# Kernel tuning notes

Hardware: AMD Instinct MI355X
Metric: run time of the kernel (lower is better)

Reference implementation:

```python
import jax, jax.numpy as jnp
import numpy as np

C = 256        # conv_dim / hidden_size
VOC = 106      # voc_size + 1
MAX_LEN = 25   # num_chars
GROUPS = 32


def setup_inputs() -> dict:
    key = jax.random.key(0)
    ks = jax.random.split(key, 32)
    s = 0.05
    d = {}
    d['rois'] = jax.random.normal(ks[0], (64, C, 16, 128), jnp.float32)
    d['conv1_w'] = jax.random.normal(ks[1], (C, C, 3, 3), jnp.float32) * s
    d['gn1_g'] = jnp.ones((C,), jnp.float32)
    d['gn1_b'] = jnp.zeros((C,), jnp.float32)
    d['conv2_w'] = jax.random.normal(ks[2], (C, C, 3, 3), jnp.float32) * s
    d['gn2_g'] = jnp.ones((C,), jnp.float32)
    d['gn2_b'] = jnp.zeros((C,), jnp.float32)
    # BiLSTM (nIn=C, nHidden=C), PyTorch gate order i,f,g,o
    d['lstm_wih_f'] = jax.random.normal(ks[3], (4 * C, C), jnp.float32) * s
    d['lstm_whh_f'] = jax.random.normal(ks[4], (4 * C, C), jnp.float32) * s
    d['lstm_bih_f'] = jnp.zeros((4 * C,), jnp.float32)
    d['lstm_bhh_f'] = jnp.zeros((4 * C,), jnp.float32)
    d['lstm_wih_b'] = jax.random.normal(ks[5], (4 * C, C), jnp.float32) * s
    d['lstm_whh_b'] = jax.random.normal(ks[6], (4 * C, C), jnp.float32) * s
    d['lstm_bih_b'] = jnp.zeros((4 * C,), jnp.float32)
    d['lstm_bhh_b'] = jnp.zeros((4 * C,), jnp.float32)
    d['emb_w'] = jax.random.normal(ks[7], (C, 2 * C), jnp.float32) * s   # 2H -> C projection
    d['emb_b'] = jnp.zeros((C,), jnp.float32)
    # Attention decoder params
    d['att_emb'] = jax.random.normal(ks[8], (VOC, C), jnp.float32) * s   # char embedding table
    d['comb_w'] = jax.random.normal(ks[9], (C, 2 * C), jnp.float32) * s  # attn_combine
    d['comb_b'] = jnp.zeros((C,), jnp.float32)
    d['gru_wih'] = jax.random.normal(ks[10], (3 * C, C), jnp.float32) * s  # gates r,z,n
    d['gru_whh'] = jax.random.normal(ks[11], (3 * C, C), jnp.float32) * s
    d['gru_bih'] = jnp.zeros((3 * C,), jnp.float32)
    d['gru_bhh'] = jnp.zeros((3 * C,), jnp.float32)
    d['out_w'] = jax.random.normal(ks[12], (VOC, C), jnp.float32) * s
    d['out_b'] = jnp.zeros((VOC,), jnp.float32)
    d['vat_w'] = jax.random.normal(ks[13], (1, C), jnp.float32) * s
    d['vat_b'] = jnp.zeros((1,), jnp.float32)
    return d


def _group_norm(x, g, b, eps=1e-5):
    N, Ch, H, W = x.shape
    xg = x.reshape(N, GROUPS, Ch // GROUPS, H, W)
    m = xg.mean(axis=(2, 3, 4), keepdims=True)
    v = xg.var(axis=(2, 3, 4), keepdims=True)
    xn = ((xg - m) / jnp.sqrt(v + eps)).reshape(N, Ch, H, W)
    return xn * g[None, :, None, None] + b[None, :, None, None]


def _conv_gn_relu(x, w, g, b):
    y = jax.lax.conv_general_dilated(x, w, window_strides=(2, 1),
                                     padding=((1, 1), (1, 1)),
                                     dimension_numbers=('NCHW', 'OIHW', 'NCHW'))
    return jax.nn.relu(_group_norm(y, g, b))


def _lstm_dir(x, Wih, Whh, bih, bhh, reverse):
    # x: (T, N, C) -> hidden states (T, N, H)
    N = x.shape[1]
    Hd = Whh.shape[1]
    def step(carry, xt):
        h, c = carry
        gates = xt @ Wih.T + h @ Whh.T + (bih + bhh)
        i, f, gg, o = jnp.split(gates, 4, axis=-1)
        c = jax.nn.sigmoid(f) * c + jax.nn.sigmoid(i) * jnp.tanh(gg)
        h = jax.nn.sigmoid(o) * jnp.tanh(c)
        return (h, c), h
    init = (jnp.zeros((N, Hd), x.dtype), jnp.zeros((N, Hd), x.dtype))
    _, hs = jax.lax.scan(step, init, x, reverse=reverse)
    return hs


def _forward(rois, conv1_w, gn1_g, gn1_b, conv2_w, gn2_g, gn2_b,
             lstm_wih_f, lstm_whh_f, lstm_bih_f, lstm_bhh_f,
             lstm_wih_b, lstm_whh_b, lstm_bih_b, lstm_bhh_b,
             emb_w, emb_b, att_emb, comb_w, comb_b,
             gru_wih, gru_whh, gru_bih, gru_bhh, out_w, out_b, vat_w, vat_b):
    # CRNN encoder
    x = _conv_gn_relu(rois, conv1_w, gn1_g, gn1_b)
    x = _conv_gn_relu(x, conv2_w, gn2_g, gn2_b)
    x = x.mean(axis=2)                      # (N, C, W)
    x = jnp.transpose(x, (2, 0, 1))         # (T, N, C)
    fw = _lstm_dir(x, lstm_wih_f, lstm_whh_f, lstm_bih_f, lstm_bhh_f, False)
    bw = _lstm_dir(x, lstm_wih_b, lstm_whh_b, lstm_bih_b, lstm_bhh_b, True)
    rec = jnp.concatenate([fw, bw], axis=-1)        # (T, N, 2C)
    enc = rec @ emb_w.T + emb_b                     # (T, N, C) encoder_outputs

    n = enc.shape[1]

    def dec_step(carry, _):
        inp, h = carry                              # inp: (n,) int, h: (n, C)
        e = att_emb[inp]                            # embedding (dropout = identity at eval)
        alpha = jnp.tanh(h[None, :, :] + enc)       # (T, n, C)
        aw = jnp.squeeze(alpha @ vat_w.T, -1) + vat_b[0]  # (T, n)
        aw = jax.nn.softmax(aw, axis=0)             # softmax over time
        ctx = jnp.einsum('tn,tnc->nc', aw, enc)     # attn_applied
        o = jax.nn.relu(jnp.concatenate([e, ctx], axis=-1) @ comb_w.T + comb_b)
        gi = o @ gru_wih.T + gru_bih
        gh = h @ gru_whh.T + gru_bhh
        ir, iz, innw = jnp.split(gi, 3, axis=-1)
        hr, hz, hn = jnp.split(gh, 3, axis=-1)
        r = jax.nn.sigmoid(ir + hr)
        z = jax.nn.sigmoid(iz + hz)
        nn_ = jnp.tanh(innw + r * hn)
        h2 = (1.0 - z) * nn_ + z * h
        logits = jax.nn.log_softmax(h2 @ out_w.T + out_b, axis=-1)
        ni = jnp.argmax(logits, axis=-1)            # greedy feedback
        return (ni, h2), logits

    init = (jnp.zeros((n,), jnp.int32), jnp.zeros((n, C), enc.dtype))
    _, outs = jax.lax.scan(dec_step, init, None, length=MAX_LEN)
    return jnp.transpose(outs, (1, 0, 2))           # decoder_raw: (n, MAX_LEN, VOC)


def reference(rois, conv1_w, gn1_g, gn1_b, conv2_w, gn2_g, gn2_b,
              lstm_wih_f, lstm_whh_f, lstm_bih_f, lstm_bhh_f,
              lstm_wih_b, lstm_whh_b, lstm_bih_b, lstm_bhh_b,
              emb_w, emb_b, att_emb, comb_w, comb_b,
              gru_wih, gru_whh, gru_bih, gru_bhh, out_w, out_b, vat_w, vat_b):
    return _forward(rois, conv1_w, gn1_g, gn1_b, conv2_w, gn2_g, gn2_b,
                    lstm_wih_f, lstm_whh_f, lstm_bih_f, lstm_bhh_f,
                    lstm_wih_b, lstm_whh_b, lstm_bih_b, lstm_bhh_b,
                    emb_w, emb_b, att_emb, comb_w, comb_b,
                    gru_wih, gru_whh, gru_bih, gru_bhh, out_w, out_b, vat_w, vat_b)
```

## Files before the change

kernel.cpp:

```cpp
#include <hip/hip_runtime.h>
#include <cstdint>

typedef unsigned short u16;
typedef unsigned int   u32;
typedef __attribute__((ext_vector_type(8))) __bf16 bf16x8;
typedef __attribute__((ext_vector_type(4))) float  f32x4;

#define DEV static __device__ __forceinline__

DEV float bf2f(u16 u) { union { u32 i; float f; } v; v.i = ((u32)u) << 16; return v.f; }
DEV u16 f2bf(float f) {
  union { float f; u32 i; } v; v.f = f;
  u32 x = v.i;
  x += 0x7fffu + ((x >> 16) & 1u);
  return (u16)(x >> 16);
}
DEV void splitf(float x, u16 &h, u16 &l) { h = f2bf(x); float r = x - bf2f(h); l = f2bf(r); }
DEV float sigm(float x) { return 1.f / (1.f + __expf(-x)); }
DEV float tanh_(float x) { float e = __expf(2.f * x); return 1.f - 2.f / (e + 1.f); }
DEV f32x4 mfma_bf16(bf16x8 a, bf16x8 b, f32x4 c) {
  return __builtin_amdgcn_mfma_f32_16x16x32_bf16(a, b, c, 0, 0, 0);
}

__global__ __launch_bounds__(256) void k_repack_convw(const float* __restrict__ w,
                                                      u16* __restrict__ oh, u16* __restrict__ ol) {
  int idx = blockIdx.x * 256 + threadIdx.x;
  if (idx >= 256 * 2304) return;
  int co = idx / 2304, r = idx - co * 2304;
  int seg = r >> 8, ci = r & 255;
  float v = w[(co * 256 + ci) * 9 + seg];
  u16 h, l; splitf(v, h, l);
  oh[idx] = h; ol[idx] = l;
}

__global__ __launch_bounds__(256) void k_split(const float* __restrict__ s,
                                               u16* __restrict__ h, u16* __restrict__ l, int count) {
  int i = blockIdx.x * 256 + threadIdx.x;
  if (i < count) { u16 a, b; splitf(s[i], a, b); h[i] = a; l[i] = b; }
}

template <int H_OUT, int H_IN, int MODE>
__global__ __launch_bounds__(256)
void k_conv_gemm(const float* __restrict__ Ain, const u16* __restrict__ Bth, const u16* __restrict__ Btl,
                 float* __restrict__ Out, const float* __restrict__ gstat,
                 const float* __restrict__ gamma, const float* __restrict__ beta) {
  __shared__ __align__(16) u16 Ash[128 * 32];
  __shared__ __align__(16) u16 Asl[128 * 32];
  __shared__ __align__(16) u16 Bsh[128 * 32];
  __shared__ __align__(16) u16 Bsl[128 * 32];
  const int tid = threadIdx.x;
  const int bx = blockIdx.x, ct = blockIdx.y;
  const int n = bx / H_OUT, hp = bx % H_OUT;
  const int wid = tid >> 6, lane = tid & 63;
  const int wr = wid >> 1, wc = wid & 1;
  const int lr = lane & 15, lk = lane >> 4;
  const int iw = tid & 127, chalf = tid >> 7;
  f32x4 acc[4][4] = {};
  for (int step = 0; step < 72; ++step) {
    const int seg = step >> 3, ci0 = (step & 7) << 5;
    const int kh = seg / 3, kw = seg - kh * 3;
    const int ih = 2 * hp + kh - 1;
    const int iws = iw + kw - 1;
    const bool ok = (ih >= 0) && (ih < H_IN) && (iws >= 0) && (iws < 128);
#pragma unroll
    for (int j = 0; j < 2; ++j) {
      int chunk = j * 256 + tid;
      int row = chunk >> 2, sub = chunk & 3;
      int off = (ct * 128 + row) * 2304 + step * 32 + sub * 8;
      *(uint4*)&Bsh[chunk * 8] = *(const uint4*)&Bth[off];
      *(uint4*)&Bsl[chunk * 8] = *(const uint4*)&Btl[off];
    }
    if constexpr (MODE == 0) {
      const float* src = Ain + (((long)(n * 256 + ci0) * H_IN + ih) * 128 + iws);
#pragma unroll
      for (int g8 = 0; g8 < 2; ++g8) {
        u32 ph[4], pl[4];
#pragma unroll
        for (int q = 0; q < 4; ++q) {
          int c = chalf * 16 + g8 * 8 + q * 2;
          float v0 = 0.f, v1 = 0.f;
          if (ok) { v0 = src[(long)c * (H_IN * 128)]; v1 = src[(long)(c + 1) * (H_IN * 128)]; }
          u16 h0, l0, h1, l1; splitf(v0, h0, l0); splitf(v1, h1, l1);
          ph[q] = (u32)h0 | ((u32)h1 << 16);
          pl[q] = (u32)l0 | ((u32)l1 << 16);
        }
        *(uint4*)&Ash[iw * 32 + chalf * 16 + g8 * 8] = make_uint4(ph[0], ph[1], ph[2], ph[3]);
        *(uint4*)&Asl[iw * 32 + chalf * 16 + g8 * 8] = make_uint4(pl[0], pl[1], pl[2], pl[3]);
      }
    } else {
      const float* src = Ain + ((((long)n * H_IN + ih) * 128 + iws) * 256 + ci0 + chalf * 16);
#pragma unroll
      for (int g8 = 0; g8 < 2; ++g8) {
        int c0 = ci0 + chalf * 16 + g8 * 8;
        int g = c0 >> 3;
        float m = gstat[(n * 32 + g) * 2], rs = gstat[(n * 32 + g) * 2 + 1];
        float x[8] = {};
        if (ok) {
          float4 a = *(const float4*)(src + g8 * 8);
          float4 b = *(const float4*)(src + g8 * 8 + 4);
          x[0] = a.x; x[1] = a.y; x[2] = a.z; x[3] = a.w;
          x[4] = b.x; x[5] = b.y; x[6] = b.z; x[7] = b.w;
        }
        u32 ph[4], pl[4];
#pragma unroll
        for (int q = 0; q < 4; ++q) {
          int c = c0 + q * 2;
          float v0 = ok ? fmaxf((x[q * 2]     - m) * rs * gamma[c]     + beta[c],     0.f) : 0.f;
          float v1 = ok ? fmaxf((x[q * 2 + 1] - m) * rs * gamma[c + 1] + beta[c + 1], 0.f) : 0.f;
          u16 h0, l0, h1, l1; splitf(v0, h0, l0); splitf(v1, h1, l1);
          ph[q] = (u32)h0 | ((u32)h1 << 16);
          pl[q] = (u32)l0 | ((u32)l1 << 16);
        }
        *(uint4*)&Ash[iw * 32 + chalf * 16 + g8 * 8] = make_uint4(ph[0], ph[1], ph[2], ph[3]);
        *(uint4*)&Asl[iw * 32 + chalf * 16 + g8 * 8] = make_uint4(pl[0], pl[1], pl[2], pl[3]);
      }
    }
    __syncthreads();
    bf16x8 ah[4], al[4], bh[4], bl[4];
#pragma unroll
    for (int mi = 0; mi < 4; ++mi) {
      int row = wr * 64 + mi * 16 + lr;
      ah[mi] = *(const bf16x8*)&Ash[row * 32 + lk * 8];
      al[mi] = *(const bf16x8*)&Asl[row * 32 + lk * 8];
    }
#pragma unroll
    for (int ni = 0; ni < 4; ++ni) {
      int row = wc * 64 + ni * 16 + lr;
      bh[ni] = *(const bf16x8*)&Bsh[row * 32 + lk * 8];
      bl[ni] = *(const bf16x8*)&Bsl[row * 32 + lk * 8];
    }
#pragma unroll
    for (int mi = 0; mi < 4; ++mi)
#pragma unroll
      for (int ni = 0; ni < 4; ++ni) {
        f32x4 c = acc[mi][ni];
        c = mfma_bf16(al[mi], bh[ni], c);
        c = mfma_bf16(ah[mi], bl[ni], c);
        c = mfma_bf16(ah[mi], bh[ni], c);
        acc[mi][ni] = c;
      }
    __syncthreads();
  }
#pragma unroll
  for (int mi = 0; mi < 4; ++mi)
#pragma unroll
    for (int ni = 0; ni < 4; ++ni)
#pragma unroll
      for (int r = 0; r < 4; ++r) {
        int w = wr * 64 + mi * 16 + lk * 4 + r;
        int co = ct * 128 + wc * 64 + ni * 16 + lr;
        Out[(((long)(n * H_OUT + hp)) * 128 + w) * 256 + co] = acc[mi][ni][r];
      }
}

__global__ __launch_bounds__(256)
void k_gemm_split(const u16* __restrict__ Ah, const u16* __restrict__ Al,
                  const u16* __restrict__ Bh, const u16* __restrict__ Bl,
                  float* __restrict__ outF, const float* __restrict__ bias, int K) {
  __shared__ __align__(16) u16 Ash[128 * 32];
  __shared__ __align__(16) u16 Asl[128 * 32];
  __shared__ __align__(16) u16 Bsh[128 * 32];
  __shared__ __align__(16) u16 Bsl[128 * 32];
  const int tid = threadIdx.x;
  const int m0 = blockIdx.x * 128, n0 = blockIdx.y * 128;
  const int N = gridDim.y * 128;
  const int wid = tid >> 6, lane = tid & 63;
  const int wr = wid >> 1, wc = wid & 1;
  const int lr = lane & 15, lk = lane >> 4;
  f32x4 acc[4][4] = {};
  const int steps = K >> 5;
  for (int s = 0; s < steps; ++s) {
    const int k0 = s << 5;
#pragma unroll
    for (int j = 0; j < 2; ++j) {
      int chunk = j * 256 + tid;
      int row = chunk >> 2, sub = chunk & 3;
      long aoff = (long)(m0 + row) * K + k0 + sub * 8;
      long boff = (long)(n0 + row) * K + k0 + sub * 8;
      *(uint4*)&Ash[chunk * 8] = *(const uint4*)&Ah[aoff];
      *(uint4*)&Asl[chunk * 8] = *(const uint4*)&Al[aoff];
      *(uint4*)&Bsh[chunk * 8] = *(const uint4*)&Bh[boff];
      *(uint4*)&Bsl[chunk * 8] = *(const uint4*)&Bl[boff];
    }
    __syncthreads();
    bf16x8 ah[4], al[4], bh[4], bl[4];
#pragma unroll
    for (int mi = 0; mi < 4; ++mi) {
      int row = wr * 64 + mi * 16 + lr;
      ah[mi] = *(const bf16x8*)&Ash[row * 32 + lk * 8];
      al[mi] = *(const bf16x8*)&Asl[row * 32 + lk * 8];
    }
#pragma unroll
    for (int ni = 0; ni < 4; ++ni) {
      int row = wc * 64 + ni * 16 + lr;
      bh[ni] = *(const bf16x8*)&Bsh[row * 32 + lk * 8];
      bl[ni] = *(const bf16x8*)&Bsl[row * 32 + lk * 8];
    }
#pragma unroll
    for (int mi = 0; mi < 4; ++mi)
#pragma unroll
      for (int ni = 0; ni < 4; ++ni) {
        f32x4 c = acc[mi][ni];
        c = mfma_bf16(al[mi], bh[ni], c);
        c = mfma_bf16(ah[mi], bl[ni], c);
        c = mfma_bf16(ah[mi], bh[ni], c);
        acc[mi][ni] = c;
      }
    __syncthreads();
  }
#pragma unroll
  for (int mi = 0; mi < 4; ++mi)
#pragma unroll
    for (int ni = 0; ni < 4; ++ni)
#pragma unroll
      for (int r = 0; r < 4; ++r) {
        int m = m0 + wr * 64 + mi * 16 + lk * 4 + r;
        int col = n0 + wc * 64 + ni * 16 + lr;
        float v = acc[mi][ni][r];
        if (bias) v += bias[col];
        outF[(long)m * N + col] = v;
      }
}

__global__ __launch_bounds__(256)
void k_gemm_gx(const u16* __restrict__ Ah, const u16* __restrict__ Al,
               const u16* __restrict__ Bh, const u16* __restrict__ Bl,
               float* __restrict__ outF) {
  __shared__ __align__(16) u16 Ash[128 * 32];
  __shared__ __align__(16) u16 Asl[128 * 32];
  __shared__ __align__(16) u16 Bsh[128 * 32];
  __shared__ __align__(16) u16 Bsl[128 * 32];
  const int tid = threadIdx.x;
  const int m0 = blockIdx.x * 128, n0 = blockIdx.y * 128;
  const int K = 256;
  const int wid = tid >> 6, lane = tid & 63;
  const int wr = wid >> 1, wc = wid & 1;
  const int lr = lane & 15, lk = lane >> 4;
  f32x4 acc[4][4] = {};
  for (int s = 0; s < 8; ++s) {
    const int k0 = s << 5;
#pragma unroll
    for (int j = 0; j < 2; ++j) {
      int chunk = j * 256 + tid;
      int row = chunk >> 2, sub = chunk & 3;
      long aoff = (long)(m0 + row) * K + k0 + sub * 8;
      long boff = (long)(n0 + row) * K + k0 + sub * 8;
      *(uint4*)&Ash[chunk * 8] = *(const uint4*)&Ah[aoff];
      *(uint4*)&Asl[chunk * 8] = *(const uint4*)&Al[aoff];
      *(uint4*)&Bsh[chunk * 8] = *(const uint4*)&Bh[boff];
      *(uint4*)&Bsl[chunk * 8] = *(const uint4*)&Bl[boff];
    }
    __syncthreads();
    bf16x8 ah[4], al[4], bh[4], bl[4];
#pragma unroll
    for (int mi = 0; mi < 4; ++mi) {
      int row = wr * 64 + mi * 16 + lr;
      ah[mi] = *(const bf16x8*)&Ash[row * 32 + lk * 8];
      al[mi] = *(const bf16x8*)&Asl[row * 32 + lk * 8];
    }
#pragma unroll
    for (int ni = 0; ni < 4; ++ni) {
      int row = wc * 64 + ni * 16 + lr;
      bh[ni] = *(const bf16x8*)&Bsh[row * 32 + lk * 8];
      bl[ni] = *(const bf16x8*)&Bsl[row * 32 + lk * 8];
    }
#pragma unroll
    for (int mi = 0; mi < 4; ++mi)
#pragma unroll
      for (int ni = 0; ni < 4; ++ni) {
        f32x4 c = acc[mi][ni];
        c = mfma_bf16(al[mi], bh[ni], c);
        c = mfma_bf16(ah[mi], bl[ni], c);
        c = mfma_bf16(ah[mi], bh[ni], c);
        acc[mi][ni] = c;
      }
    __syncthreads();
  }
#pragma unroll
  for (int mi = 0; mi < 4; ++mi)
#pragma unroll
    for (int ni = 0; ni < 4; ++ni) {
      int t = blockIdx.x * 2 + wr;
      int nbase = mi * 16 + lk * 4;
      int col = n0 + wc * 64 + ni * 16 + lr;
      int gate = col >> 8, u = col & 255;
      int prow = ((u >> 4) << 6) + (gate << 4) + (u & 15);
      float4 st = make_float4(acc[mi][ni][0], acc[mi][ni][1], acc[mi][ni][2], acc[mi][ni][3]);
      *(float4*)&outF[((long)t * 1024 + prow) * 64 + nbase] = st;
    }
}

__global__ __launch_bounds__(256)
void k_gn_stats(const float* __restrict__ y, float* __restrict__ stat, int H) {
  const int n = blockIdx.x >> 5, g = blockIdx.x & 31;
  const int tid = threadIdx.x;
  const int cnt = H * 128;
  float s = 0.f, q = 0.f;
  for (int i = tid; i < cnt; i += 256) {
    int h = i >> 7, w = i & 127;
    const float4* p = (const float4*)(y + (((long)(n * H + h) * 128 + w) * 256 + g * 8));
    float4 a = p[0], b = p[1];
    s += a.x + a.y + a.z + a.w + b.x + b.y + b.z + b.w;
    q += a.x * a.x + a.y * a.y + a.z * a.z + a.w * a.w + b.x * b.x + b.y * b.y + b.z * b.z + b.w * b.w;
  }
  __shared__ float rs_[256], rq_[256];
  rs_[tid] = s; rq_[tid] = q; __syncthreads();
  for (int off = 128; off > 0; off >>= 1) {
    if (tid < off) { rs_[tid] += rs_[tid + off]; rq_[tid] += rq_[tid + off]; }
    __syncthreads();
  }
  if (tid == 0) {
    float c = (float)(cnt * 8);
    float m = rs_[0] / c;
    float var = rq_[0] / c - m * m;
    stat[(n * 32 + g) * 2] = m;
    stat[(n * 32 + g) * 2 + 1] = rsqrtf(var + 1e-5f);
  }
}

__global__ __launch_bounds__(256)
void k_xbuild(const float* __restrict__ out2, const float* __restrict__ stat,
              const float* __restrict__ gamma, const float* __restrict__ beta,
              u16* __restrict__ xh, u16* __restrict__ xl) {
  int idx = blockIdx.x * 256 + threadIdx.x;
  int c = idx & 255;
  int n = (idx >> 8) & 63;
  int t = idx >> 14;
  int g = c >> 3;
  float m = stat[(n * 32 + g) * 2], rs = stat[(n * 32 + g) * 2 + 1];
  float ga = gamma[c], be = beta[c];
  float acc = 0.f;
#pragma unroll
  for (int h = 0; h < 4; ++h) {
    float v = out2[(((long)(n * 4 + h) * 128 + t) * 256) + c];
    acc += fmaxf((v - m) * rs * ga + be, 0.f);
  }
  acc *= 0.25f;
  u16 a, b; splitf(acc, a, b);
  xh[idx] = a; xl[idx] = b;
}

__global__ __launch_bounds__(256)
void k_lstm_mfma(const float* __restrict__ gxPf, const float* __restrict__ gxPb,
                 const float* __restrict__ whhf, const float* __restrict__ whhb,
                 const float* __restrict__ bihf, const float* __restrict__ bhhf,
                 const float* __restrict__ bihb, const float* __restrict__ bhhb,
                 u16* __restrict__ hHi, u16* __restrict__ hLo,
                 u16* __restrict__ hsH, u16* __restrict__ hsL,
                 int* __restrict__ bar) {
  __shared__ __align__(16) u16 WH[128 * 256];
  __shared__ __align__(16) u16 WL[128 * 256];
  const int tid = threadIdx.x;
  const int dir = blockIdx.x >> 3;
  const int b   = blockIdx.x & 7;
  const float* whh = dir ? whhb : whhf;
  const float* bih = dir ? bihb : bihf;
  const float* bhh = dir ? bhhb : bhhf;
  const float* gxP = dir ? gxPb : gxPf;
  for (int i = tid; i < 8192; i += 256) {
    int r = i >> 6;
    int kc = (i & 63) << 2;
    int gate = r >> 5, uu = r & 31;
    const float* src = whh + ((long)(gate * 256 + b * 32 + uu)) * 256 + kc;
    float4 v = *(const float4*)src;
    u16 h0, l0, h1, l1, h2, l2, h3, l3;
    splitf(v.x, h0, l0); splitf(v.y, h1, l1); splitf(v.z, h2, l2); splitf(v.w, h3, l3);
    int byte = (r << 9) + (kc << 1);
    byte ^= (r & 7) << 4;
    *(ushort4*)((char*)WH + byte) = make_ushort4(h0, h1, h2, h3);
    *(ushort4*)((char*)WL + byte) = make_ushort4(l0, l1, l2, l3);
  }
  const int wid = tid >> 6, lane = tid & 63;
  const int lr = lane & 15, lk = lane >> 4;
  const int n0 = wid * 16;
  float bias_[2][4];
#pragma unroll
  for (int uh = 0; uh < 2; ++uh)
#pragma unroll
    for (int g = 0; g < 4; ++g) {
      int row = g * 256 + b * 32 + uh * 16 + lr;
      bias_[uh][g] = bih[row] + bhh[row];
    }
  float creg[2][4] = {};
  const char* WHc = (const char*)WH;
  const char* WLc = (const char*)WL;
  float4 gxc[2][4];
  {
    const int t0 = dir ? 127 : 0;
#pragma unroll
    for (int uh = 0; uh < 2; ++uh)
#pragma unroll
      for (int g = 0; g < 4; ++g)
        gxc[uh][g] = *(const float4*)&gxP[((size_t)t0 * 1024 + (b * 2 + uh) * 64 + g * 16 + lr) * 64 + n0 + lk * 4];
  }
  __syncthreads();
  for (int s = 0; s < 128; ++s) {
    const int t = dir ? (127 - s) : s;
    const int rb = s & 1, wb = rb ^ 1;
    const u16* hrH = hHi + (size_t)((rb * 2 + dir) * 64) * 256;
    const u16* hrL = hLo + (size_t)((rb * 2 + dir) * 64) * 256;
    f32x4 acc[8] = {};
#pragma unroll
    for (int ks = 0; ks < 8; ++ks) {
      bf16x8 ah = *(const bf16x8*)&hrH[(n0 + lr) * 256 + ks * 32 + lk * 8];
      bf16x8 al = *(const bf16x8*)&hrL[(n0 + lr) * 256 + ks * 32 + lk * 8];
#pragma unroll
      for (int ni = 0; ni < 8; ++ni) {
        int byte = ((ni * 16 + lr) << 9) + (ks << 6) + (lk << 4);
        byte ^= (lr & 7) << 4;
        bf16x8 bh = *(const bf16x8*)(WHc + byte);
        bf16x8 bl = *(const bf16x8*)(WLc + byte);
        f32x4 c = acc[ni];
        c = mfma_bf16(al, bh, c);
        c = mfma_bf16(ah, bl, c);
        c = mfma_bf16(ah, bh, c);
        acc[ni] = c;
      }
    }
    float4 gxn[2][4];
    if (s < 127) {
      const int tn = dir ? (126 - s) : (s + 1);
#pragma unroll
      for (int uh = 0; uh < 2; ++uh)
#pragma unroll
        for (int g = 0; g < 4; ++g)
          gxn[uh][g] = *(const float4*)&gxP[((size_t)tn * 1024 + (b * 2 + uh) * 64 + g * 16 + lr) * 64 + n0 + lk * 4];
    }
    u16* hwH = hHi + (size_t)((wb * 2 + dir) * 64) * 256;
    u16* hwL = hLo + (size_t)((wb * 2 + dir) * 64) * 256;
#pragma unroll
    for (int uh = 0; uh < 2; ++uh) {
      const int u = b * 32 + uh * 16 + lr;
#pragma unroll
      for (int r = 0; r < 4; ++r) {
        float iv = sigm(acc[0 * 2 + uh][r] + ((const float*)&gxc[uh][0])[r] + bias_[uh][0]);
        float fv = sigm(acc[1 * 2 + uh][r] + ((const float*)&gxc[uh][1])[r] + bias_[uh][1]);
        float gv = tanh_(acc[2 * 2 + uh][r] + ((const float*)&gxc[uh][2])[r] + bias_[uh][2]);
        float ov = sigm(acc[3 * 2 + uh][r] + ((const float*)&gxc[uh][3])[r] + bias_[uh][3]);
        creg[uh][r] = fv * creg[uh][r] + iv * gv;
        float hv = ov * tanh_(creg[uh][r]);
        u16 hh, hl; splitf(hv, hh, hl);
        int n = n0 + lk * 4 + r;
        hwH[n * 256 + u] = hh;
        hwL[n * 256 + u] = hl;
        size_t o = ((size_t)(t * 64 + n)) * 512 + dir * 256 + u;
        hsH[o] = hh; hsL[o] = hl;
      }
    }
    if (s < 127) {
#pragma unroll
      for (int uh = 0; uh < 2; ++uh)
#pragma unroll
        for (int g = 0; g < 4; ++g)
          gxc[uh][g] = gxn[uh][g];
    }
    __syncthreads();
    if (tid == 0) {
      __hip_atomic_fetch_add(&bar[dir], 1, __ATOMIC_ACQ_REL, __HIP_MEMORY_SCOPE_AGENT);
      const int target = (s + 1) * 8;
      while (__hip_atomic_load(&bar[dir], __ATOMIC_RELAXED, __HIP_MEMORY_SCOPE_AGENT) < target)
        __builtin_amdgcn_s_sleep(1);
    }
    __syncthreads();
    __threadfence();
  }
}

__global__ __launch_bounds__(1024)
void k_decoder(const float* __restrict__ enc, const float* __restrict__ att_emb,
               const float* __restrict__ comb_w, const float* __restrict__ comb_b,
               const float* __restrict__ gru_wih, const float* __restrict__ gru_whh,
               const float* __restrict__ gru_bih, const float* __restrict__ gru_bhh,
               const float* __restrict__ out_w, const float* __restrict__ out_b,
               const float* __restrict__ vat_w, float* __restrict__ dout) {
  const int n = blockIdx.x, tid = threadIdx.x;
  __shared__ float hsh[256], esh[256], ctx[256], osh[256], vsh[256];
  __shared__ float sc[128], lg[128];
  __shared__ float part[1024];
  __shared__ float gp[1536];
  __shared__ float op[1024];
  __shared__ float sca[2];
  __shared__ int inp_sh;
  if (tid < 256) { hsh[tid] = 0.f; vsh[tid] = vat_w[tid]; }
  if (tid == 0) inp_sh = 0;
  __syncthreads();
  for (int step = 0; step < 25; ++step) {
    if (tid < 256) esh[tid] = att_emb[inp_sh * 256 + tid];
    {
      const int t = tid >> 3, kq = tid & 7;
      const float* ep = enc + ((t * 64 + n) * 256 + kq * 32);
      const float* hp = hsh + kq * 32;
      const float* vp = vsh + kq * 32;
      float a = 0.f;
#pragma unroll
      for (int k0 = 0; k0 < 32; ++k0) {
        int k = (k0 + kq * 4) & 31;
        a += tanh_(hp[k] + ep[k]) * vp[k];
      }
      a += __shfl_xor(a, 1); a += __shfl_xor(a, 2); a += __shfl_xor(a, 4);
      if (kq == 0) sc[t] = a;
    }
    __syncthreads();
    if (tid < 64) {
      float v0 = sc[tid], v1 = sc[tid + 64];
      float m = fmaxf(v0, v1);
      for (int w = 1; w < 64; w <<= 1) m = fmaxf(m, __shfl_xor(m, w));
      float e0 = __expf(v0 - m), e1 = __expf(v1 - m);
      sc[tid] = e0; sc[tid + 64] = e1;
      float ss = e0 + e1;
      for (int w = 1; w < 64; w <<= 1) ss += __shfl_xor(ss, w);
      if (tid == 0) sca[0] = 1.f / ss;
    }
    __syncthreads();
    const float sinv = sca[0];
    {
      const int c = tid & 255, tq = tid >> 8;
      const float* ep = enc + (((tq * 32) * 64 + n) * 256 + c);
      float a = 0.f;
#pragma unroll 4
      for (int t2 = 0; t2 < 32; ++t2) a += sc[tq * 32 + t2] * ep[(size_t)t2 * 16384];
      part[tq * 256 + c] = a;
    }
    __syncthreads();
    if (tid < 256) ctx[tid] = (part[tid] + part[256 + tid] + part[512 + tid] + part[768 + tid]) * sinv;
    __syncthreads();
    {
      const int u = tid & 255, kq = tid >> 8;
      const float* w = comb_w + (size_t)u * 512 + kq * 128;
      const float* src = (kq < 2) ? (esh + kq * 128) : (ctx + (kq - 2) * 128);
      float a = 0.f;
      for (int k = 0; k < 128; k += 4) {
        float4 wv = *(const float4*)(w + k);
        a += src[k] * wv.x + src[k + 1] * wv.y + src[k + 2] * wv.z + src[k + 3] * wv.w;
      }
      part[kq * 256 + u] = a;
    }
    __syncthreads();
    if (tid < 256)
      osh[tid] = fmaxf(part[tid] + part[256 + tid] + part[512 + tid] + part[768 + tid] + comb_b[tid], 0.f);
    __syncthreads();
    {
      const int u = tid & 255, m = tid >> 8;
      const float* w1; const float* s1;
      if (m == 0)      { w1 = gru_wih + (size_t)u * 256;         s1 = osh; }
      else if (m == 1) { w1 = gru_wih + (size_t)(256 + u) * 256; s1 = osh; }
      else if (m == 2) { w1 = gru_wih + (size_t)(512 + u) * 256; s1 = osh; }
      else             { w1 = gru_whh + (size_t)u * 256;         s1 = hsh; }
      float a = 0.f;
      for (int k = 0; k < 256; k += 4) {
        float4 wv = *(const float4*)(w1 + k);
        a += s1[k] * wv.x + s1[k + 1] * wv.y + s1[k + 2] * wv.z + s1[k + 3] * wv.w;
      }
      gp[m * 256 + u] = a;
      if (m < 2) {
        const float* w2 = gru_whh + (size_t)((m + 1) * 256 + u) * 256;
        float a2 = 0.f;
        for (int k = 0; k < 256; k += 4) {
          float4 wv = *(const float4*)(w2 + k);
          a2 += hsh[k] * wv.x + hsh[k + 1] * wv.y + hsh[k + 2] * wv.z + hsh[k + 3] * wv.w;
        }
        gp[(4 + m) * 256 + u] = a2;
      }
    }
    __syncthreads();
    if (tid < 256) {
      float r  = sigm(gp[tid] + gru_bih[tid] + gp[768 + tid] + gru_bhh[tid]);
      float z  = sigm(gp[256 + tid] + gru_bih[256 + tid] + gp[1024 + tid] + gru_bhh[256 + tid]);
      float nn = tanh_(gp[512 + tid] + gru_bih[512 + tid] + r * (gp[1280 + tid] + gru_bhh[512 + tid]));
      hsh[tid] = (1.f - z) * nn + z * hsh[tid];
    }
    __syncthreads();
    {
      const int u = tid & 127, kq = tid >> 7;
      float a = 0.f;
      if (u < 106) {
        const float* w = out_w + (size_t)u * 256 + kq * 32;
        const float* hp = hsh + kq * 32;
        for (int k = 0; k < 32; k += 4) {
          float4 wv = *(const float4*)(w + k);
          a += hp[k] * wv.x + hp[k + 1] * wv.y + hp[k + 2] * wv.z + hp[k + 3] * wv.w;
        }
      }
      op[kq * 128 + u] = a;
    }
    __syncthreads();
    if (tid < 128) {
      float a = op[tid] + op[128 + tid] + op[256 + tid] + op[384 + tid]
              + op[512 + tid] + op[640 + tid] + op[768 + tid] + op[896 + tid];
      lg[tid] = (tid < 106) ? (a + out_b[tid]) : -3.0e38f;
    }
    __syncthreads();
    if (tid < 64) {
      float v0 = lg[tid];
      float v1 = lg[tid + 64];
      float m; int im;
      if (v1 > v0) { m = v1; im = tid + 64; } else { m = v0; im = tid; }
      for (int w = 1; w < 64; w <<= 1) {
        float mo = __shfl_xor(m, w); int io = __shfl_xor(im, w);
        if (mo > m || (mo == m && io < im)) { m = mo; im = io; }
      }
      float e = __expf(v0 - m) + ((tid + 64 < 106) ? __expf(v1 - m) : 0.f);
      for (int w = 1; w < 64; w <<= 1) e += __shfl_xor(e, w);
      if (tid == 0) { sca[0] = m + __logf(e); inp_sh = im; }
    }
    __syncthreads();
    if (tid < 106) dout[((size_t)n * 25 + step) * 106 + tid] = lg[tid] - sca[0];
    __syncthreads();
  }
}

extern "C" void kernel_launch(void* const* d_in, const int* in_sizes, int n_in,
                              void* d_out, int out_size, void* d_ws, size_t ws_size,
                              hipStream_t stream) {
  (void)in_sizes; (void)n_in; (void)out_size;
  const float* rois    = (const float*)d_in[0];
  const float* conv1_w = (const float*)d_in[1];
  const float* gn1_g   = (const float*)d_in[2];
  const float* gn1_b   = (const float*)d_in[3];
  const float* conv2_w = (const float*)d_in[4];
  const float* gn2_g   = (const float*)d_in[5];
  const float* gn2_b   = (const float*)d_in[6];
  const float* wih_f   = (const float*)d_in[7];
  const float* whh_f   = (const float*)d_in[8];
  const float* bih_f   = (const float*)d_in[9];
  const float* bhh_f   = (const float*)d_in[10];
  const float* wih_b   = (const float*)d_in[11];
  const float* whh_b   = (const float*)d_in[12];
  const float* bih_b   = (const float*)d_in[13];
  const float* bhh_b   = (const float*)d_in[14];
  const float* emb_w   = (const float*)d_in[15];
  const float* emb_b   = (const float*)d_in[16];
  const float* att_emb = (const float*)d_in[17];
  const float* comb_w  = (const float*)d_in[18];
  const float* comb_b  = (const float*)d_in[19];
  const float* gru_wih = (const float*)d_in[20];
  const float* gru_whh = (const float*)d_in[21];
  const float* gru_bih = (const float*)d_in[22];
  const float* gru_bhh = (const float*)d_in[23];
  const float* out_w   = (const float*)d_in[24];
  const float* out_b   = (const float*)d_in[25];
  const float* vat_w   = (const float*)d_in[26];

  if (ws_size < 116686864u) return;
  char* ws = (char*)d_ws;
  float* OUT1  = (float*)(ws + 0);
  float* GXF   = (float*)(ws + 0);
  float* GXB   = (float*)(ws + 33554432);
  float* OUT2  = (float*)(ws + 67108864);
  u16*   HSH_  = (u16*)  (ws + 67108864);
  u16*   HSL_  = (u16*)  (ws + 75497472);
  float* ENC   = (float*)(ws + 83886080);
  u16*   XBH   = (u16*)  (ws + 100663296);
  u16*   XBL   = (u16*)  (ws + 104857600);
  u16*   W1TH  = (u16*)  (ws + 109051904);
  u16*   W1TL  = (u16*)  (ws + 110231552);
  u16*   W2TH  = (u16*)  (ws + 111411200);
  u16*   W2TL  = (u16*)  (ws + 112590848);
  u16*   WIHFH = (u16*)  (ws + 113770496);
  u16*   WIHFL = (u16*)  (ws + 114294784);
  u16*   WIHBH = (u16*)  (ws + 114819072);
  u16*   WIHBL = (u16*)  (ws + 115343360);
  u16*   EMBWH = (u16*)  (ws + 115867648);
  u16*   EMBWL = (u16*)  (ws + 116129792);
  float* GN1S  = (float*)(ws + 116391936);
  float* GN2S  = (float*)(ws + 116408320);
  u16*   HBUFH = (u16*)  (ws + 116424704);
  u16*   HBUFL = (u16*)  (ws + 116555776);
  int*   BAR   = (int*)  (ws + 116686848);

  hipMemsetAsync(HBUFH, 0, 131072, stream);
  hipMemsetAsync(HBUFL, 0, 131072, stream);
  hipMemsetAsync(BAR, 0, 16, stream);

  k_repack_convw<<<2304, 256, 0, stream>>>(conv1_w, W1TH, W1TL);
  k_repack_convw<<<2304, 256, 0, stream>>>(conv2_w, W2TH, W2TL);
  k_split<<<1024, 256, 0, stream>>>(wih_f, WIHFH, WIHFL, 262144);
  k_split<<<1024, 256, 0, stream>>>(wih_b, WIHBH, WIHBL, 262144);
  k_split<<<512, 256, 0, stream>>>(emb_w, EMBWH, EMBWL, 131072);

  k_conv_gemm<8, 16, 0><<<dim3(512, 2), 256, 0, stream>>>(rois, W1TH, W1TL, OUT1, nullptr, nullptr, nullptr);
  k_gn_stats<<<2048, 256, 0, stream>>>(OUT1, GN1S, 8);
  k_conv_gemm<4, 8, 1><<<dim3(256, 2), 256, 0, stream>>>(OUT1, W2TH, W2TL, OUT2, GN1S, gn1_g, gn1_b);
  k_gn_stats<<<2048, 256, 0, stream>>>(OUT2, GN2S, 4);
  k_xbuild<<<8192, 256, 0, stream>>>(OUT2, GN2S, gn2_g, gn2_b, XBH, XBL);

  k_gemm_gx<<<dim3(64, 8), 256, 0, stream>>>(XBH, XBL, WIHFH, WIHFL, GXF);
  k_gemm_gx<<<dim3(64, 8), 256, 0, stream>>>(XBH, XBL, WIHBH, WIHBL, GXB);
  k_lstm_mfma<<<16, 256, 0, stream>>>(GXF, GXB, whh_f, whh_b, bih_f, bhh_f, bih_b, bhh_b,
                                      HBUFH, HBUFL, HSH_, HSL_, BAR);
  k_gemm_split<<<dim3(64, 2), 256, 0, stream>>>(HSH_, HSL_, EMBWH, EMBWL, ENC, emb_b, 512);

  k_decoder<<<64, 1024, 0, stream>>>(ENC, att_emb, comb_w, comb_b, gru_wih, gru_whh,
                                     gru_bih, gru_bhh, out_w, out_b, vat_w, (float*)d_out);
}
```

Before: 4.218 ms.

## Restructure attention decoder as cooperative grid with global barriers sharing weight GEMVs

Measured after the change: 8.491 ms. 2.01x slower.

```diff
diff --git a/kernel.cpp b/kernel.cpp
--- a/kernel.cpp
+++ b/kernel.cpp
@@ -20,6 +20,17 @@
 DEV float tanh_(float x) { float e = __expf(2.f * x); return 1.f - 2.f / (e + 1.f); }
 DEV f32x4 mfma_bf16(bf16x8 a, bf16x8 b, f32x4 c) {
   return __builtin_amdgcn_mfma_f32_16x16x32_bf16(a, b, c, 0, 0, 0);
+}
+
+DEV void gbar(int* flags, int tag) {
+  __syncthreads();
+  if (threadIdx.x == 0)
+    __hip_atomic_store(&flags[blockIdx.x * 32], tag, __ATOMIC_RELEASE, __HIP_MEMORY_SCOPE_AGENT);
+  if (threadIdx.x < 64) {
+    while (__hip_atomic_load(&flags[threadIdx.x * 32], __ATOMIC_ACQUIRE, __HIP_MEMORY_SCOPE_AGENT) < tag)
+      __builtin_amdgcn_s_sleep(1);
+  }
+  __syncthreads();
 }
 
 __global__ __launch_bounds__(256) void k_repack_convw(const float* __restrict__ w,
@@ -466,146 +477,146 @@
   }
 }
 
-__global__ __launch_bounds__(1024)
-void k_decoder(const float* __restrict__ enc, const float* __restrict__ att_emb,
-               const float* __restrict__ comb_w, const float* __restrict__ comb_b,
-               const float* __restrict__ gru_wih, const float* __restrict__ gru_whh,
-               const float* __restrict__ gru_bih, const float* __restrict__ gru_bhh,
-               const float* __restrict__ out_w, const float* __restrict__ out_b,
-               const float* __restrict__ vat_w, float* __restrict__ dout) {
-  const int n = blockIdx.x, tid = threadIdx.x;
-  __shared__ float hsh[256], esh[256], ctx[256], osh[256], vsh[256];
-  __shared__ float sc[128], lg[128];
-  __shared__ float part[1024];
-  __shared__ float gp[1536];
-  __shared__ float op[1024];
-  __shared__ float sca[2];
-  __shared__ int inp_sh;
-  if (tid < 256) { hsh[tid] = 0.f; vsh[tid] = vat_w[tid]; }
-  if (tid == 0) inp_sh = 0;
-  __syncthreads();
+__global__ __launch_bounds__(256)
+void k_decoder_coop(const float* __restrict__ enc, const float* __restrict__ att_emb,
+                    const float* __restrict__ comb_w, const float* __restrict__ comb_b,
+                    const float* __restrict__ gru_wih, const float* __restrict__ gru_whh,
+                    const float* __restrict__ gru_bih, const float* __restrict__ gru_bhh,
+                    const float* __restrict__ out_w, const float* __restrict__ out_b,
+                    const float* __restrict__ vat_w, float* __restrict__ dout,
+                    int* __restrict__ flags, int* __restrict__ inp,
+                    float* __restrict__ H, float* __restrict__ HT,
+                    float* __restrict__ ECT, float* __restrict__ O_,
+                    float* __restrict__ GH_, float* __restrict__ GI_) {
+  const int b = blockIdx.x, tid = threadIdx.x;
+  const int wv = tid >> 6, lane = tid & 63;
+  __shared__ float p_lds[128];
+  __shared__ float h2_lds[256];
+  __shared__ float op_lds[256];
+  __shared__ float sca[1];
+  int tag = 0;
   for (int step = 0; step < 25; ++step) {
-    if (tid < 256) esh[tid] = att_emb[inp_sh * 256 + tid];
     {
-      const int t = tid >> 3, kq = tid & 7;
-      const float* ep = enc + ((t * 64 + n) * 256 + kq * 32);
-      const float* hp = hsh + kq * 32;
-      const float* vp = vsh + kq * 32;
+      const int n = b;
+      const int ip = inp[n];
+      ECT[tid * 64 + n] = att_emb[ip * 256 + tid];
+      const float4 h4 = *(const float4*)&H[n * 256 + lane * 4];
+      const float4 v4 = *(const float4*)&vat_w[lane * 4];
+      for (int i = 0; i < 32; ++i) {
+        const int t = i * 4 + wv;
+        const float4 e4 = *(const float4*)&enc[(size_t)(t * 64 + n) * 256 + lane * 4];
+        float s = tanh_(h4.x + e4.x) * v4.x + tanh_(h4.y + e4.y) * v4.y
+                + tanh_(h4.z + e4.z) * v4.z + tanh_(h4.w + e4.w) * v4.w;
+        s += __shfl_xor(s, 1); s += __shfl_xor(s, 2); s += __shfl_xor(s, 4);
+        s += __shfl_xor(s, 8); s += __shfl_xor(s, 16); s += __shfl_xor(s, 32);
+        if (lane == 0) p_lds[t] = s;
+      }
+      __syncthreads();
+      if (tid < 64) {
+        float v0 = p_lds[tid], v1 = p_lds[tid + 64];
+        float m = fmaxf(v0, v1);
+        for (int w = 1; w < 64; w <<= 1) m = fmaxf(m, __shfl_xor(m, w));
+        float e0 = __expf(v0 - m), e1 = __expf(v1 - m);
+        p_lds[tid] = e0; p_lds[tid + 64] = e1;
+        float ss = e0 + e1;
+        for (int w = 1; w < 64; w <<= 1) ss += __shfl_xor(ss, w);
+        if (tid == 0) sca[0] = 1.f / ss;
+      }
+      __syncthreads();
+      const float sinv = sca[0];
+      float acc = 0.f;
+      for (int t = 0; t < 128; t += 4) {
+        acc += p_lds[t]     * enc[(size_t)((t)     * 64 + n) * 256 + tid];
+        acc += p_lds[t + 1] * enc[(size_t)((t + 1) * 64 + n) * 256 + tid];
+        acc += p_lds[t + 2] * enc[(size_t)((t + 2) * 64 + n) * 256 + tid];
+        acc += p_lds[t + 3] * enc[(size_t)((t + 3) * 64 + n) * 256 + tid];
+      }
+      ECT[(256 + tid) * 64 + n] = acc * sinv;
+    }
+    gbar(flags, ++tag);
+    if (b < 16) {
+      const int u0 = b * 16 + wv * 4;
+      const float* w0 = comb_w + (size_t)u0 * 512;
+      float a0 = 0.f, a1 = 0.f, a2 = 0.f, a3 = 0.f;
+#pragma unroll 4
+      for (int k = 0; k < 512; ++k) {
+        float x = ECT[k * 64 + lane];
+        a0 += x * w0[k]; a1 += x * w0[512 + k]; a2 += x * w0[1024 + k]; a3 += x * w0[1536 + k];
+      }
+      O_[(u0 + 0) * 64 + lane] = fmaxf(a0 + comb_b[u0 + 0], 0.f);
+      O_[(u0 + 1) * 64 + lane] = fmaxf(a1 + comb_b[u0 + 1], 0.f);
+      O_[(u0 + 2) * 64 + lane] = fmaxf(a2 + comb_b[u0 + 2], 0.f);
+      O_[(u0 + 3) * 64 + lane] = fmaxf(a3 + comb_b[u0 + 3], 0.f);
+    } else if (b < 32) {
+      const int r0 = (b - 16) * 48 + wv * 12;
+      const float* w0 = gru_whh + (size_t)r0 * 256;
+      float acc[12] = {};
+#pragma unroll 2
+      for (int k = 0; k < 256; ++k) {
+        float x = HT[k * 64 + lane];
+#pragma unroll
+        for (int j = 0; j < 12; ++j) acc[j] += x * w0[(size_t)j * 256 + k];
+      }
+#pragma unroll
+      for (int j = 0; j < 12; ++j) GH_[(r0 + j) * 64 + lane] = acc[j];
+    }
+    gbar(flags, ++tag);
+    {
+      const int r0 = b * 12 + wv * 3;
+      const float* w0 = gru_wih + (size_t)r0 * 256;
+      float a0 = 0.f, a1 = 0.f, a2 = 0.f;
+#pragma unroll 4
+      for (int k = 0; k < 256; ++k) {
+        float x = O_[k * 64 + lane];
+        a0 += x * w0[k]; a1 += x * w0[256 + k]; a2 += x * w0[512 + k];
+      }
+      GI_[(r0 + 0) * 64 + lane] = a0;
+      GI_[(r0 + 1) * 64 + lane] = a1;
+      GI_[(r0 + 2) * 64 + lane] = a2;
+    }
+    gbar(flags, ++tag);
+    {
+      const int n = b;
+      const float gir = GI_[tid * 64 + n], giz = GI_[(256 + tid) * 64 + n], gin = GI_[(512 + tid) * 64 + n];
+      const float ghr = GH_[tid * 64 + n], ghz = GH_[(256 + tid) * 64 + n], ghn = GH_[(512 + tid) * 64 + n];
+      const float r = sigm(gir + gru_bih[tid] + ghr + gru_bhh[tid]);
+      const float z = sigm(giz + gru_bih[256 + tid] + ghz + gru_bhh[256 + tid]);
+      const float nn = tanh_(gin + gru_bih[512 + tid] + r * (ghn + gru_bhh[512 + tid]));
+      const float h2 = (1.f - z) * nn + z * H[n * 256 + tid];
+      H[n * 256 + tid] = h2;
+      HT[tid * 64 + n] = h2;
+      h2_lds[tid] = h2;
+      __syncthreads();
+      const int v = tid & 127, kq = tid >> 7;
       float a = 0.f;
-#pragma unroll
-      for (int k0 = 0; k0 < 32; ++k0) {
-        int k = (k0 + kq * 4) & 31;
-        a += tanh_(hp[k] + ep[k]) * vp[k];
-      }
-      a += __shfl_xor(a, 1); a += __shfl_xor(a, 2); a += __shfl_xor(a, 4);
-      if (kq == 0) sc[t] = a;
-    }
-    __syncthreads();
-    if (tid < 64) {
-      float v0 = sc[tid], v1 = sc[tid + 64];
-      float m = fmaxf(v0, v1);
-      for (int w = 1; w < 64; w <<= 1) m = fmaxf(m, __shfl_xor(m, w));
-      float e0 = __expf(v0 - m), e1 = __expf(v1 - m);
-      sc[tid] = e0; sc[tid + 64] = e1;
-      float ss = e0 + e1;
-      for (int w = 1; w < 64; w <<= 1) ss += __shfl_xor(ss, w);
-      if (tid == 0) sca[0] = 1.f / ss;
-    }
-    __syncthreads();
-    const float sinv = sca[0];
-    {
-      const int c = tid & 255, tq = tid >> 8;
-      const float* ep = enc + (((tq * 32) * 64 + n) * 256 + c);
-      float a = 0.f;
-#pragma unroll 4
-      for (int t2 = 0; t2 < 32; ++t2) a += sc[tq * 32 + t2] * ep[(size_t)t2 * 16384];
-      part[tq * 256 + c] = a;
-    }
-    __syncthreads();
-    if (tid < 256) ctx[tid] = (part[tid] + part[256 + tid] + part[512 + tid] + part[768 + tid]) * sinv;
-    __syncthreads();
-    {
-      const int u = tid & 255, kq = tid >> 8;
-      const float* w = comb_w + (size_t)u * 512 + kq * 128;
-      const float* src = (kq < 2) ? (esh + kq * 128) : (ctx + (kq - 2) * 128);
-      float a = 0.f;
-      for (int k = 0; k < 128; k += 4) {
-        float4 wv = *(const float4*)(w + k);
-        a += src[k] * wv.x + src[k + 1] * wv.y + src[k + 2] * wv.z + src[k + 3] * wv.w;
-      }
-      part[kq * 256 + u] = a;
-    }
-    __syncthreads();
-    if (tid < 256)
-      osh[tid] = fmaxf(part[tid] + part[256 + tid] + part[512 + tid] + part[768 + tid] + comb_b[tid], 0.f);
-    __syncthreads();
-    {
-      const int u = tid & 255, m = tid >> 8;
-      const float* w1; const float* s1;
-      if (m == 0)      { w1 = gru_wih + (size_t)u * 256;         s1 = osh; }
-      else if (m == 1) { w1 = gru_wih + (size_t)(256 + u) * 256; s1 = osh; }
-      else if (m == 2) { w1 = gru_wih + (size_t)(512 + u) * 256; s1 = osh; }
-      else             { w1 = gru_whh + (size_t)u * 256;         s1 = hsh; }
-      float a = 0.f;
-      for (int k = 0; k < 256; k += 4) {
-        float4 wv = *(const float4*)(w1 + k);
-        a += s1[k] * wv.x + s1[k + 1] * wv.y + s1[k + 2] * wv.z + s1[k + 3] * wv.w;
-      }
-      gp[m * 256 + u] = a;
-      if (m < 2) {
-        const float* w2 = gru_whh + (size_t)((m + 1) * 256 + u) * 256;
-        float a2 = 0.f;
-        for (int k = 0; k < 256; k += 4) {
-          float4 wv = *(const float4*)(w2 + k);
-          a2 += hsh[k] * wv.x + hsh[k + 1] * wv.y + hsh[k + 2] * wv.z + hsh[k + 3] * wv.w;
+      if (v < 106) {
+        const float* w = out_w + (size_t)v * 256 + kq * 128;
+        const float* hp = h2_lds + kq * 128;
+        for (int k = 0; k < 128; k += 4) {
+          a += hp[k] * w[k] + hp[k + 1] * w[k + 1] + hp[k + 2] * w[k + 2] + hp[k + 3] * w[k + 3];
         }
-        gp[(4 + m) * 256 + u] = a2;
-      }
-    }
-    __syncthreads();
-    if (tid < 256) {
-      float r  = sigm(gp[tid] + gru_bih[tid] + gp[768 + tid] + gru_bhh[tid]);
-      float z  = sigm(gp[256 + tid] + gru_bih[256 + tid] + gp[1024 + tid] + gru_bhh[256 + tid]);
-      float nn = tanh_(gp[512 + tid] + gru_bih[512 + tid] + r * (gp[1280 + tid] + gru_bhh[512 + tid]));
-      hsh[tid] = (1.f - z) * nn + z * hsh[tid];
-    }
-    __syncthreads();
-    {
-      const int u = tid & 127, kq = tid >> 7;
-      float a = 0.f;
-      if (u < 106) {
-        const float* w = out_w + (size_t)u * 256 + kq * 32;
-        const float* hp = hsh + kq * 32;
-        for (int k = 0; k < 32; k += 4) {
-          float4 wv = *(const float4*)(w + k);
-          a += hp[k] * wv.x + hp[k + 1] * wv.y + hp[k + 2] * wv.z + hp[k + 3] * wv.w;
+      }
+      op_lds[tid] = a;
+      __syncthreads();
+      if (tid < 128)
+        p_lds[tid] = (tid < 106) ? (op_lds[tid] + op_lds[128 + tid] + out_b[tid]) : -3.0e38f;
+      __syncthreads();
+      if (tid < 64) {
+        float v0 = p_lds[tid], v1 = p_lds[tid + 64];
+        float m; int im;
+        if (v1 > v0) { m = v1; im = tid + 64; } else { m = v0; im = tid; }
+        for (int w = 1; w < 64; w <<= 1) {
+          float mo = __shfl_xor(m, w); int io = __shfl_xor(im, w);
+          if (mo > m || (mo == m && io < im)) { m = mo; im = io; }
         }
-      }
-      op[kq * 128 + u] = a;
-    }
-    __syncthreads();
-    if (tid < 128) {
-      float a = op[tid] + op[128 + tid] + op[256 + tid] + op[384 + tid]
-              + op[512 + tid] + op[640 + tid] + op[768 + tid] + op[896 + tid];
-      lg[tid] = (tid < 106) ? (a + out_b[tid]) : -3.0e38f;
-    }
-    __syncthreads();
-    if (tid < 64) {
-      float v0 = lg[tid];
-      float v1 = lg[tid + 64];
-      float m; int im;
-      if (v1 > v0) { m = v1; im = tid + 64; } else { m = v0; im = tid; }
-      for (int w = 1; w < 64; w <<= 1) {
-        float mo = __shfl_xor(m, w); int io = __shfl_xor(im, w);
-        if (mo > m || (mo == m && io < im)) { m = mo; im = io; }
-      }
-      float e = __expf(v0 - m) + ((tid + 64 < 106) ? __expf(v1 - m) : 0.f);
-      for (int w = 1; w < 64; w <<= 1) e += __shfl_xor(e, w);
-      if (tid == 0) { sca[0] = m + __logf(e); inp_sh = im; }
-    }
-    __syncthreads();
-    if (tid < 106) dout[((size_t)n * 25 + step) * 106 + tid] = lg[tid] - sca[0];
-    __syncthreads();
+        float e = __expf(v0 - m) + ((tid + 64 < 106) ? __expf(v1 - m) : 0.f);
+        for (int w = 1; w < 64; w <<= 1) e += __shfl_xor(e, w);
+        if (tid == 0) { sca[0] = m + __logf(e); inp[n] = im; }
+      }
+      __syncthreads();
+      if (tid < 106) dout[((size_t)n * 25 + step) * 106 + tid] = p_lds[tid] - sca[0];
+      __syncthreads();
+    }
   }
 }
 
@@ -668,6 +679,16 @@
   u16*   HBUFL = (u16*)  (ws + 116555776);
   int*   BAR   = (int*)  (ws + 116686848);
 
+  char* dbase = ws + 100663296;
+  int*   DFLG = (int*)  (dbase + 0);
+  int*   DINP = (int*)  (dbase + 8192);
+  float* DH   = (float*)(dbase + 16384);
+  float* DHT  = (float*)(dbase + 81920);
+  float* DECT = (float*)(dbase + 147456);
+  float* DO_  = (float*)(dbase + 278528);
+  float* DGH  = (float*)(dbase + 344064);
+  float* DGI  = (float*)(dbase + 540672);
+
   hipMemsetAsync(HBUFH, 0, 131072, stream);
   hipMemsetAsync(HBUFL, 0, 131072, stream);
   hipMemsetAsync(BAR, 0, 16, stream);
@@ -686,10 +707,12 @@
 
   k_gemm_gx<<<dim3(64, 8), 256, 0, stream>>>(XBH, XBL, WIHFH, WIHFL, GXF);
   k_gemm_gx<<<dim3(64, 8), 256, 0, stream>>>(XBH, XBL, WIHBH, WIHBL, GXB);
+  hipMemsetAsync(dbase, 0, 147456, stream);
   k_lstm_mfma<<<16, 256, 0, stream>>>(GXF, GXB, whh_f, whh_b, bih_f, bhh_f, bih_b, bhh_b,
                                       HBUFH, HBUFL, HSH_, HSL_, BAR);
   k_gemm_split<<<dim3(64, 2), 256, 0, stream>>>(HSH_, HSL_, EMBWH, EMBWL, ENC, emb_b, 512);
 
-  k_decoder<<<64, 1024, 0, stream>>>(ENC, att_emb, comb_w, comb_b, gru_wih, gru_whh,
-                                     gru_bih, gru_bhh, out_w, out_b, vat_w, (float*)d_out);
-}
+  k_decoder_coop<<<64, 256, 0, stream>>>(ENC, att_emb, comb_w, comb_b, gru_wih, gru_whh,
+                                         gru_bih, gru_bhh, out_w, out_b, vat_w, (float*)d_out,
+                                         DFLG, DINP, DH, DHT, DECT, DO_, DGH, DGI);
+}
```
